# Optimization experiments

Measured on AMD Instinct MI355X. Metric: run time of the kernel, lower is better.

Reference implementation:

```python
import jax, jax.numpy as jnp
import numpy as np

D_KQ = 1024  # output_key_query_dim, used for the 1/sqrt(d) scale


def setup_inputs() -> dict:
    key = jax.random.key(0)
    kx, kq, kk, kv = jax.random.split(key, 4)
    B, S, D = 4, 2048, 1024
    x = jax.random.normal(kx, (B, S, D), dtype=jnp.float32)
    # nn.Linear(in, out, bias=False) weights, shape (out, in); y = x @ W.T
    scale = 1.0 / np.sqrt(D)
    Wq = jax.random.normal(kq, (D_KQ, D), dtype=jnp.float32) * scale
    Wk = jax.random.normal(kk, (D_KQ, D), dtype=jnp.float32) * scale
    Wv = jax.random.normal(kv, (D, D), dtype=jnp.float32) * scale
    return {"x": x, "Wq": Wq, "Wk": Wk, "Wv": Wv}


def reference(x, Wq, Wk, Wv):
    # q, k, v projections (bias=False): y = x @ W.T
    q = jnp.einsum('bsd,ed->bse', x, Wq)  # [B,S,Dkq]
    k = jnp.einsum('bsd,ed->bse', x, Wk)  # [B,S,Dkq]
    v = jnp.einsum('bsd,ed->bse', x, Wv)  # [B,S,Dv]
    scores = jnp.einsum('bqe,bke->bqk', q, k) / jnp.sqrt(
        jnp.asarray(D_KQ, dtype=q.dtype))
    # NOTE: the original torch code's masked_fill(causal_mask == 1, -inf) is a
    # no-op because the buffer contains only {-inf, 0} values, never 1.
    # Faithfully, NO causal mask is applied.
    attn = jax.nn.softmax(scores, axis=-1)
    # dropout in eval mode -> identity
    out = jnp.einsum('bqk,bke->bqe', attn, v)  # [B,S,Dv]
    return out
```

## Files before the change

### kernel.cpp

```cpp
#include <hip/hip_runtime.h>
#include <stdint.h>

#define B_ 4
#define S_ 2048
#define D_ 1024

typedef __attribute__((ext_vector_type(8))) short short8;
typedef __attribute__((ext_vector_type(4))) float f32x4;
typedef __attribute__((ext_vector_type(4))) int int4v;

__device__ inline ushort f2bf(float f) {
  union { float f; uint32_t u; } v; v.f = f;
  uint32_t u = v.u;
  u += 0x7FFFu + ((u >> 16) & 1u);
  return (ushort)(u >> 16);
}

__device__ inline float bf2f(ushort u) {
  union { uint32_t u; float f; } c; c.u = ((uint32_t)u) << 16;
  return c.f;
}

__device__ inline void gload_lds16(const ushort* g, ushort* l) {
  __builtin_amdgcn_global_load_lds(
      (__attribute__((address_space(1))) void*)(uintptr_t)g,
      (__attribute__((address_space(3))) void*)(uintptr_t)l,
      16, 0, 0);
}

__device__ inline uint lds_off(const ushort* p) {
  return (uint)(uintptr_t)(const __attribute__((address_space(3))) ushort*)(uintptr_t)p;
}

__device__ inline short8 dsr128(uint addr) {
  int4v r;
  asm volatile("ds_read_b128 %0, %1" : "=v"(r) : "v"(addr));
  return __builtin_bit_cast(short8, r);
}

__device__ inline void vwaitN(int n) {
  switch (n) {
    case 0: asm volatile("s_waitcnt vmcnt(0)"); break;
    case 1: asm volatile("s_waitcnt vmcnt(1)"); break;
    case 2: asm volatile("s_waitcnt vmcnt(2)"); break;
    case 3: asm volatile("s_waitcnt vmcnt(3)"); break;
    case 4: asm volatile("s_waitcnt vmcnt(4)"); break;
    case 5: asm volatile("s_waitcnt vmcnt(5)"); break;
    case 6: asm volatile("s_waitcnt vmcnt(6)"); break;
    case 7: asm volatile("s_waitcnt vmcnt(7)"); break;
    default: asm volatile("s_waitcnt vmcnt(8)"); break;
  }
}

__device__ inline void abar() { asm volatile("s_barrier"); }

__device__ inline void lgkm0() {
  asm volatile("s_waitcnt lgkmcnt(0)");
  __builtin_amdgcn_sched_barrier(0);
}

__global__ __launch_bounds__(256) void convert_all(
    const float* __restrict__ x, const float* __restrict__ wq,
    const float* __restrict__ wk, const float* __restrict__ wv,
    ushort* __restrict__ xb, ushort* __restrict__ wcat) {
  const int NX = B_ * S_ * D_;
  const int NW = D_ * D_;
  int e = (blockIdx.x * 256 + threadIdx.x) * 4;
  const float* src;
  ushort* dst;
  if (e < NX) {
    src = x + e; dst = xb + e;
  } else {
    int e2 = e - NX;
    int w = e2 / NW, off = e2 - w * NW;
    src = (w == 0 ? wq : w == 1 ? wk : wv) + off;
    dst = wcat + e2;
  }
  float4 f = *(const float4*)src;
  ushort4 o;
  o.x = f2bf(f.x); o.y = f2bf(f.y); o.z = f2bf(f.z); o.w = f2bf(f.w);
  *(ushort4*)dst = o;
}

template <int HH, int NH>
__device__ inline void mfma16(short8 (&af)[4][2], short8 (&bf)[2][2][2],
                              f32x4 (&acc)[8][4]) {
  __builtin_amdgcn_s_setprio(1);
  #pragma unroll
  for (int mf = 0; mf < 4; ++mf)
    #pragma unroll
    for (int nf = 0; nf < 2; ++nf)
      #pragma unroll
      for (int ks = 0; ks < 2; ++ks)
        acc[HH * 4 + mf][NH * 2 + nf] = __builtin_amdgcn_mfma_f32_16x16x32_bf16(
            af[mf][ks], bf[NH][nf][ks], acc[HH * 4 + mf][NH * 2 + nf], 0, 0, 0);
  __builtin_amdgcn_s_setprio(0);
}

__global__ __launch_bounds__(512, 2) void gemm256(
    const ushort* __restrict__ A, const ushort* __restrict__ Bm,
    ushort* __restrict__ C, int K, int lda, int ldb, int ldc,
    long sA, long sB, long sC, float scale) {
  constexpr int ATILE = 256 * 64;
  __shared__ ushort lds[4 * ATILE];
  ushort* ldsA = lds;
  ushort* ldsB = lds + 2 * ATILE;

  const int tid = threadIdx.x;
  const int wid = tid >> 6, lane = tid & 63;
  const int wr = wid >> 2, wc = wid & 3;
  const int la = lane & 15, kg = lane >> 4;
  const int m0 = blockIdx.x * 256, n0 = blockIdx.y * 256;
  const int bz = blockIdx.z;
  const ushort* Ag = A + (size_t)bz * sA;
  const ushort* Bg = Bm + (size_t)bz * sB;

  uint aOff[2][2]; int aDst[2][2];
  uint bOff[2][2]; int bDst[2][2];
  #pragma unroll
  for (int h = 0; h < 2; ++h)
    #pragma unroll
    for (int l = 0; l < 2; ++l) {
      int li = l * 512 + tid, ridx = li >> 3, c = li & 7;
      int rowA = (ridx < 64) ? h * 64 + ridx : 128 + h * 64 + (ridx - 64);
      int gcA = c ^ (rowA & 7);
      aOff[h][l] = (uint)((m0 + rowA) * lda + gcA * 8);
      aDst[h][l] = rowA * 64 + c * 8;
      int rowB = (ridx >> 5) * 64 + h * 32 + (ridx & 31);
      int gcB = c ^ (rowB & 7);
      bOff[h][l] = (uint)((n0 + rowB) * ldb + gcB * 8);
      bDst[h][l] = rowB * 64 + c * 8;
    }

  auto stageA = [&](int h, int buf, int t) {
    #pragma unroll
    for (int l = 0; l < 2; ++l)
      gload_lds16(Ag + aOff[h][l] + (size_t)t * 64, ldsA + buf * ATILE + aDst[h][l]);
  };
  auto stageB = [&](int h, int buf, int t) {
    #pragma unroll
    for (int l = 0; l < 2; ++l)
      gload_lds16(Bg + bOff[h][l] + (size_t)t * 64, ldsB + buf * ATILE + bDst[h][l]);
  };

  uint offAq[2][2][4];
  #pragma unroll
  for (int hh = 0; hh < 2; ++hh)
    #pragma unroll
    for (int ks = 0; ks < 2; ++ks)
      #pragma unroll
      for (int mf = 0; mf < 4; ++mf) {
        int row = wr * 128 + hh * 64 + mf * 16 + la;
        int kc = ((ks * 4 + kg) ^ (row & 7)) * 8;
        offAq[hh][ks][mf] = (uint)((row * 64 + kc) * 2);
      }
  uint offBq[2][2][2];
  #pragma unroll
  for (int nh = 0; nh < 2; ++nh)
    #pragma unroll
    for (int ks = 0; ks < 2; ++ks)
      #pragma unroll
      for (int nf = 0; nf < 2; ++nf) {
        int row = wc * 64 + nh * 32 + nf * 16 + la;
        int kc = ((ks * 4 + kg) ^ (row & 7)) * 8;
        offBq[nh][ks][nf] = (uint)((row * 64 + kc) * 2);
      }
  const uint ldsA0 = lds_off(ldsA);
  const uint ldsB0 = lds_off(ldsB);

  f32x4 acc[8][4];
  #pragma unroll
  for (int m = 0; m < 8; ++m)
    #pragma unroll
    for (int n = 0; n < 4; ++n) acc[m][n] = (f32x4)(0.f);
  short8 af[4][2];
  short8 bf[2][2][2];

  const int NT = K / 64;

  stageA(0, 0, 0); stageB(0, 0, 0); stageB(1, 0, 0); stageA(1, 0, 0);

  for (int t = 0; t < NT; ++t) {
    const uint aB = ldsA0 + (uint)((t & 1) * ATILE * 2);
    const uint bB = ldsB0 + (uint)((t & 1) * ATILE * 2);
    const int nb = (t + 1) & 1;

    vwaitN(4);
    abar();
    #pragma unroll
    for (int mf = 0; mf < 4; ++mf)
      #pragma unroll
      for (int ks = 0; ks < 2; ++ks) af[mf][ks] = dsr128(aB + offAq[0][ks][mf]);
    #pragma unroll
    for (int nf = 0; nf < 2; ++nf)
      #pragma unroll
      for (int ks = 0; ks < 2; ++ks) bf[0][nf][ks] = dsr128(bB + offBq[0][ks][nf]);
    if (t + 1 < NT) stageA(0, nb, t + 1);
    lgkm0();
    mfma16<0, 0>(af, bf, acc);

    vwaitN(t + 1 < NT ? 4 : 2);
    abar();
    #pragma unroll
    for (int nf = 0; nf < 2; ++nf)
      #pragma unroll
      for (int ks = 0; ks < 2; ++ks) bf[1][nf][ks] = dsr128(bB + offBq[1][ks][nf]);
    if (t + 1 < NT) stageB(0, nb, t + 1);
    lgkm0();
    mfma16<0, 1>(af, bf, acc);

    vwaitN(t + 1 < NT ? 4 : 0);
    abar();
    #pragma unroll
    for (int mf = 0; mf < 4; ++mf)
      #pragma unroll
      for (int ks = 0; ks < 2; ++ks) af[mf][ks] = dsr128(aB + offAq[1][ks][mf]);
    if (t + 1 < NT) stageB(1, nb, t + 1);
    lgkm0();
    mfma16<1, 0>(af, bf, acc);

    if (t + 1 < NT) stageA(1, nb, t + 1);
    mfma16<1, 1>(af, bf, acc);
  }

  #pragma unroll
  for (int mf = 0; mf < 8; ++mf) {
    #pragma unroll
    for (int nf = 0; nf < 4; ++nf) {
      int r = m0 + wr * 128 + (mf >> 2) * 64 + (mf & 3) * 16 + kg * 4;
      int col = n0 + wc * 64 + (nf >> 1) * 32 + (nf & 1) * 16 + la;
      #pragma unroll
      for (int jj = 0; jj < 4; ++jj)
        C[(size_t)bz * sC + (size_t)(r + jj) * ldc + col] =
            f2bf(acc[mf][nf][jj] * scale);
    }
  }
}

template <int H, int BM, int BN>
__device__ inline void mfma_ph(short8 (&afv)[BM / 64], short8 (&bfv)[BN / 64],
                               f32x4 (&acc)[BM / 32][BN / 64]) {
  constexpr int J = BM / 64, NF = BN / 64;
  __builtin_amdgcn_s_setprio(1);
  #pragma unroll
  for (int j = 0; j < J; ++j)
    #pragma unroll
    for (int nf = 0; nf < NF; ++nf)
      acc[H * J + j][nf] = __builtin_amdgcn_mfma_f32_16x16x32_bf16(
          afv[j], bfv[nf], acc[H * J + j][nf], 0, 0, 0);
  __builtin_amdgcn_s_setprio(0);
}

template <int BM, int BN, bool OUT_BF16, bool V_TRANS>
__global__ __launch_bounds__(512, 2) void gemm_p(
    const ushort* __restrict__ A, const ushort* __restrict__ Bm,
    void* __restrict__ C, ushort* __restrict__ Vt,
    int N, int K, int lda, int ldb, int ldc,
    long sA, long sB, long sC, float scale) {
  constexpr int J = BM / 64, NF = BN / 64, MF = BM / 32;
  constexpr int LAH = BM / 128;
  constexpr int LBH = BN / 128;
  constexpr int ABUF = BM * 64;
  constexpr int BBUF = BN * 64;
  constexpr int VW1 = 2 * LAH + 2 * LBH;
  __shared__ ushort lds[2 * ABUF + 3 * BBUF];
  ushort* ldsA = lds;
  ushort* ldsB = lds + 2 * ABUF;

  const int tid = threadIdx.x;
  const int wid = tid >> 6, lane = tid & 63;
  const int wr = wid >> 2, wc = wid & 3;
  const int la = lane & 15, kg = lane >> 4;
  const int m0 = blockIdx.x * BM, n0 = blockIdx.y * BN;
  const int bz = blockIdx.z;
  const ushort* Ag = A + (size_t)bz * sA;
  const ushort* Bg = Bm + (size_t)bz * sB;

  uint aOff[2][LAH]; int aDst[2][LAH];
  #pragma unroll
  for (int h = 0; h < 2; ++h)
    #pragma unroll
    for (int l = 0; l < LAH; ++l) {
      int li = l * 512 + tid, ridx = li >> 3, c = li & 7;
      int row = (ridx < BM / 4) ? h * (BM / 4) + ridx
                                : (h + 2) * (BM / 4) + (ridx - BM / 4);
      int gc = c ^ (row & 7);
      aOff[h][l] = (uint)((m0 + row) * lda + gc * 8);
      aDst[h][l] = row * 64 + c * 8;
    }
  uint bOff[2][LBH]; int bDst[2][LBH];
  #pragma unroll
  for (int h = 0; h < 2; ++h)
    #pragma unroll
    for (int l = 0; l < LBH; ++l) {
      int li = l * 512 + tid, ridx = li >> 3, c = li & 7;
      int row = h * (BN / 2) + ridx;
      int gc = c ^ (row & 7);
      bOff[h][l] = (uint)((n0 + row) * ldb + gc * 8);
      bDst[h][l] = row * 64 + c * 8;
    }

  auto stageA = [&](int h, int buf, int t) {
    #pragma unroll
    for (int l = 0; l < LAH; ++l)
      gload_lds16(Ag + aOff[h][l] + (size_t)t * 64, ldsA + buf * ABUF + aDst[h][l]);
  };
  auto stageB = [&](int h, int slot, int t) {
    #pragma unroll
    for (int l = 0; l < LBH; ++l)
      gload_lds16(Bg + bOff[h][l] + (size_t)t * 64, ldsB + slot * BBUF + bDst[h][l]);
  };

  uint offA[2][2][J];
  #pragma unroll
  for (int h = 0; h < 2; ++h)
    #pragma unroll
    for (int ks = 0; ks < 2; ++ks)
      #pragma unroll
      for (int j = 0; j < J; ++j) {
        int row = wr * (BM / 2) + h * (BM / 4) + j * 16 + la;
        int kc = ((ks * 4 + kg) ^ (row & 7)) * 8;
        offA[h][ks][j] = (uint)((row * 64 + kc) * 2);
      }
  uint offB[2][NF];
  #pragma unroll
  for (int ks = 0; ks < 2; ++ks)
    #pragma unroll
    for (int nf = 0; nf < NF; ++nf) {
      int row = wc * (BN / 4) + nf * 16 + la;
      int kc = ((ks * 4 + kg) ^ (row & 7)) * 8;
      offB[ks][nf] = (uint)((row * 64 + kc) * 2);
    }
  const uint ldsA0 = lds_off(ldsA);
  const uint ldsB0 = lds_off(ldsB);

  f32x4 acc[MF][NF];
  #pragma unroll
  for (int m = 0; m < MF; ++m)
    #pragma unroll
    for (int n = 0; n < NF; ++n) acc[m][n] = (f32x4)(0.f);
  short8 af[J], bf0[NF], bf1[NF];

  const int NT = K / 64;

  stageA(0, 0, 0); stageB(0, 0, 0); stageB(1, 0, 0);
  stageA(1, 0, 0);
  stageA(0, 1, 1); stageB(0, 1, 1); stageB(1, 1, 1);

  int bs = 0;
  for (int t = 0; t < NT; ++t) {
    const uint aB = ldsA0 + (uint)((t & 1) * ABUF * 2);
    const uint bB = ldsB0 + (uint)(bs * BBUF * 2);
    const int bs2 = (bs == 0) ? 2 : bs - 1;

    vwaitN(t + 1 < NT ? VW1 : LAH);
    abar();
    #pragma unroll
    for (int j = 0; j < J; ++j) af[j] = dsr128(aB + offA[0][0][j]);
    #pragma unroll
    for (int nf = 0; nf < NF; ++nf) bf0[nf] = dsr128(bB + offB[0][nf]);
    if (t + 1 < NT) stageA(1, (t + 1) & 1, t + 1);
    lgkm0();
    mfma_ph<0, BM, BN>(af, bf0, acc);
    #pragma unroll
    for (int j = 0; j < J; ++j) af[j] = dsr128(aB + offA[0][1][j]);
    #pragma unroll
    for (int nf = 0; nf < NF; ++nf) bf1[nf] = dsr128(bB + offB[1][nf]);
    lgkm0();
    mfma_ph<0, BM, BN>(af, bf1, acc);

    vwaitN(t + 1 < NT ? VW1 : 0);
    abar();
    #pragma unroll
    for (int j = 0; j < J; ++j) af[j] = dsr128(aB + offA[1][0][j]);
    if (t + 2 < NT) { stageA(0, t & 1, t + 2); stageB(0, bs2, t + 2); }
    lgkm0();
    mfma_ph<1, BM, BN>(af, bf0, acc);
    #pragma unroll
    for (int j = 0; j < J; ++j) af[j] = dsr128(aB + offA[1][1][j]);
    if (t + 2 < NT) stageB(1, bs2, t + 2);
    lgkm0();
    mfma_ph<1, BM, BN>(af, bf1, acc);

    bs = (bs == 2) ? 0 : bs + 1;
  }

  if (V_TRANS && n0 >= 2048) {
    const int b = m0 >> 11;
    ushort* Vb = Vt + (size_t)b * D_ * S_;
    #pragma unroll
    for (int m = 0; m < MF; ++m) {
      #pragma unroll
      for (int n = 0; n < NF; ++n) {
        int r = m0 + wr * (BM / 2) + m * 16 + kg * 4;
        int e = (n0 - 2048) + wc * (BN / 4) + n * 16 + la;
        int s0 = r & 2047;
        ushort4 o;
        o.x = f2bf(acc[m][n][0]); o.y = f2bf(acc[m][n][1]);
        o.z = f2bf(acc[m][n][2]); o.w = f2bf(acc[m][n][3]);
        *(ushort4*)&Vb[(size_t)e * S_ + s0] = o;
      }
    }
  } else {
    char* Cb = (char*)C;
    #pragma unroll
    for (int m = 0; m < MF; ++m) {
      #pragma unroll
      for (int n = 0; n < NF; ++n) {
        int r = m0 + wr * (BM / 2) + m * 16 + kg * 4;
        int col = n0 + wc * (BN / 4) + n * 16 + la;
        #pragma unroll
        for (int jj = 0; jj < 4; ++jj) {
          float v = acc[m][n][jj] * scale;
          size_t idx = (size_t)bz * sC + (size_t)(r + jj) * ldc + col;
          if (OUT_BF16) ((ushort*)Cb)[idx] = f2bf(v);
          else          ((float*)Cb)[idx]  = v;
        }
      }
    }
  }
}

__global__ __launch_bounds__(256) void softmax_rows(
    const ushort* __restrict__ Sc, ushort* __restrict__ P) {
  size_t row = blockIdx.x;
  const ushort* src = Sc + row * S_;
  ushort* dst = P + row * S_;
  int tid = threadIdx.x;
  short8 v = *(const short8*)(src + tid * 8);
  float vals[8];
  float m = -1e30f;
  #pragma unroll
  for (int i = 0; i < 8; ++i) {
    vals[i] = bf2f((ushort)v[i]);
    m = fmaxf(m, vals[i]);
  }
  #pragma unroll
  for (int off = 1; off < 64; off <<= 1) m = fmaxf(m, __shfl_xor(m, off));
  __shared__ float redm[4];
  if ((tid & 63) == 0) redm[tid >> 6] = m;
  __syncthreads();
  m = fmaxf(fmaxf(redm[0], redm[1]), fmaxf(redm[2], redm[3]));
  float s = 0.f;
  #pragma unroll
  for (int i = 0; i < 8; ++i) {
    vals[i] = __expf(vals[i] - m);
    s += vals[i];
  }
  #pragma unroll
  for (int off = 1; off < 64; off <<= 1) s += __shfl_xor(s, off);
  __shared__ float reds[4];
  if ((tid & 63) == 0) reds[tid >> 6] = s;
  __syncthreads();
  s = reds[0] + reds[1] + reds[2] + reds[3];
  float inv = 1.0f / s;
  short8 o;
  #pragma unroll
  for (int i = 0; i < 8; ++i) o[i] = (short)f2bf(vals[i] * inv);
  *(short8*)(dst + tid * 8) = o;
}

extern "C" void kernel_launch(void* const* d_in, const int* in_sizes, int n_in,
                              void* d_out, int out_size, void* d_ws, size_t ws_size,
                              hipStream_t stream) {
  const float* x  = (const float*)d_in[0];
  const float* Wq = (const float*)d_in[1];
  const float* Wk = (const float*)d_in[2];
  const float* Wv = (const float*)d_in[3];
  float* out = (float*)d_out;

  char* ws = (char*)d_ws;
  ushort* Xb   = (ushort*)(ws + 0);
  ushort* Wcat = (ushort*)(ws + 16777216);
  ushort* QKV  = (ushort*)(ws + 23068672);
  ushort* Vt   = (ushort*)(ws + 73400320);
  ushort* Sc   = (ushort*)(ws + 90177536);
  ushort* P    = (ushort*)(ws + 157286400);

  const int NTOT = B_ * S_ * D_ + 3 * D_ * D_;

  convert_all<<<NTOT / 4 / 256, 256, 0, stream>>>(x, Wq, Wk, Wv, Xb, Wcat);

  gemm_p<128, 256, true, true><<<dim3(64, 12, 1), 512, 0, stream>>>(
      Xb, Wcat, QKV, Vt, 3072, 1024, 1024, 1024, 3072, 0, 0, 0, 1.0f);

  gemm256<<<dim3(8, 8, B_), 512, 0, stream>>>(
      QKV, QKV + 1024, Sc, 1024, 3072, 3072, 2048,
      (long)S_ * 3072, (long)S_ * 3072, (long)S_ * S_, 1.0f / 32.0f);

  softmax_rows<<<B_ * S_, 256, 0, stream>>>(Sc, P);

  gemm_p<128, 256, false, false><<<dim3(16, 4, B_), 512, 0, stream>>>(
      P, Vt, out, nullptr, 1024, 2048, 2048, 2048, 1024,
      (long)S_ * S_, (long)S_ * D_, (long)S_ * D_, 1.0f);
}
```

Before: 168.3 us.

## Fuse softmax exp and row sums into QK^T epilogue, normalize in PV epilogue

Removes the standalone softmax kernel. The QK^T GEMM epilogue now writes exp(score) directly and produces per-tile partial row sums. The PV GEMM sums those partials and scales its output by the reciprocal. The QKV projection is also split into a gemm256 launch for Q/K and a gemm_p launch that writes only the transposed V. This avoids a full read and write of the score matrix, but it drops the max subtraction, so large scores could overflow for inputs with a larger range.

Result: faster. 156.5 us (-7.0%).

```diff
diff --git a/kernel.cpp b/kernel.cpp
--- a/kernel.cpp
+++ b/kernel.cpp
@@ -14,11 +14,6 @@
   uint32_t u = v.u;
   u += 0x7FFFu + ((u >> 16) & 1u);
   return (ushort)(u >> 16);
-}
-
-__device__ inline float bf2f(ushort u) {
-  union { uint32_t u; float f; } c; c.u = ((uint32_t)u) << 16;
-  return c.f;
 }
 
 __device__ inline void gload_lds16(const ushort* g, ushort* l) {
@@ -97,9 +92,11 @@
   __builtin_amdgcn_s_setprio(0);
 }
 
+template <bool SM>
 __global__ __launch_bounds__(512, 2) void gemm256(
     const ushort* __restrict__ A, const ushort* __restrict__ Bm,
-    ushort* __restrict__ C, int K, int lda, int ldb, int ldc,
+    ushort* __restrict__ C, float* __restrict__ psum,
+    int K, int lda, int ldb, int ldc,
     long sA, long sB, long sC, float scale) {
   constexpr int ATILE = 256 * 64;
   __shared__ ushort lds[4 * ATILE];
@@ -223,16 +220,53 @@
     mfma16<1, 1>(af, bf, acc);
   }
 
-  #pragma unroll
-  for (int mf = 0; mf < 8; ++mf) {
-    #pragma unroll
-    for (int nf = 0; nf < 4; ++nf) {
-      int r = m0 + wr * 128 + (mf >> 2) * 64 + (mf & 3) * 16 + kg * 4;
-      int col = n0 + wc * 64 + (nf >> 1) * 32 + (nf & 1) * 16 + la;
-      #pragma unroll
-      for (int jj = 0; jj < 4; ++jj)
-        C[(size_t)bz * sC + (size_t)(r + jj) * ldc + col] =
-            f2bf(acc[mf][nf][jj] * scale);
+  if constexpr (SM) {
+    __shared__ float psum_lds[4][256];
+    float rsum[8][4];
+    #pragma unroll
+    for (int mf = 0; mf < 8; ++mf)
+      #pragma unroll
+      for (int jj = 0; jj < 4; ++jj) rsum[mf][jj] = 0.f;
+    #pragma unroll
+    for (int mf = 0; mf < 8; ++mf) {
+      #pragma unroll
+      for (int nf = 0; nf < 4; ++nf) {
+        int r = m0 + wr * 128 + (mf >> 2) * 64 + (mf & 3) * 16 + kg * 4;
+        int col = n0 + wc * 64 + (nf >> 1) * 32 + (nf & 1) * 16 + la;
+        #pragma unroll
+        for (int jj = 0; jj < 4; ++jj) {
+          float e = __expf(acc[mf][nf][jj] * scale);
+          C[(size_t)bz * sC + (size_t)(r + jj) * ldc + col] = f2bf(e);
+          rsum[mf][jj] += e;
+        }
+      }
+    }
+    #pragma unroll
+    for (int mf = 0; mf < 8; ++mf)
+      #pragma unroll
+      for (int jj = 0; jj < 4; ++jj) {
+        float s = rsum[mf][jj];
+        s += __shfl_xor(s, 1); s += __shfl_xor(s, 2);
+        s += __shfl_xor(s, 4); s += __shfl_xor(s, 8);
+        if (la == 0)
+          psum_lds[wc][wr * 128 + (mf >> 2) * 64 + (mf & 3) * 16 + kg * 4 + jj] = s;
+      }
+    __syncthreads();
+    if (tid < 256)
+      psum[((size_t)bz * 8 + blockIdx.y) * 2048 + m0 + tid] =
+          psum_lds[0][tid] + psum_lds[1][tid] + psum_lds[2][tid] + psum_lds[3][tid];
+  } else {
+    #pragma unroll
+    for (int mf = 0; mf < 8; ++mf) {
+      #pragma unroll
+      for (int nf = 0; nf < 4; ++nf) {
+        int r = m0 + wr * 128 + (mf >> 2) * 64 + (mf & 3) * 16 + kg * 4;
+        int col = n0 + wc * 64 + (nf >> 1) * 32 + (nf & 1) * 16 + la;
+        #pragma unroll
+        for (int jj = 0; jj < 4; ++jj)
+          C[(size_t)bz * sC + (size_t)(r + jj) * ldc + col] =
+              f2bf(acc[mf][nf][jj] * scale);
+      }
     }
   }
 }
@@ -251,10 +285,11 @@
   __builtin_amdgcn_s_setprio(0);
 }
 
-template <int BM, int BN, bool OUT_BF16, bool V_TRANS>
+template <int BM, int BN, bool OUT_BF16, bool V_TRANS, bool NORM>
 __global__ __launch_bounds__(512, 2) void gemm_p(
     const ushort* __restrict__ A, const ushort* __restrict__ Bm,
     void* __restrict__ C, ushort* __restrict__ Vt,
+    const float* __restrict__ psum,
     int N, int K, int lda, int ldb, int ldc,
     long sA, long sB, long sC, float scale) {
   constexpr int J = BM / 64, NF = BN / 64, MF = BM / 32;
@@ -385,7 +420,20 @@
     bs = (bs == 2) ? 0 : bs + 1;
   }
 
-  if (V_TRANS && n0 >= 2048) {
+  __shared__ float inv_l[BM];
+  if constexpr (NORM) {
+    __syncthreads();
+    if (tid < BM) {
+      float s = 0.f;
+      #pragma unroll
+      for (int q = 0; q < 8; ++q)
+        s += psum[((size_t)bz * 8 + q) * 2048 + m0 + tid];
+      inv_l[tid] = 1.0f / s;
+    }
+    __syncthreads();
+  }
+
+  if constexpr (V_TRANS) {
     const int b = m0 >> 11;
     ushort* Vb = Vt + (size_t)b * D_ * S_;
     #pragma unroll
@@ -393,7 +441,7 @@
       #pragma unroll
       for (int n = 0; n < NF; ++n) {
         int r = m0 + wr * (BM / 2) + m * 16 + kg * 4;
-        int e = (n0 - 2048) + wc * (BN / 4) + n * 16 + la;
+        int e = n0 + wc * (BN / 4) + n * 16 + la;
         int s0 = r & 2047;
         ushort4 o;
         o.x = f2bf(acc[m][n][0]); o.y = f2bf(acc[m][n][1]);
@@ -407,57 +455,19 @@
     for (int m = 0; m < MF; ++m) {
       #pragma unroll
       for (int n = 0; n < NF; ++n) {
-        int r = m0 + wr * (BM / 2) + m * 16 + kg * 4;
+        int rl = wr * (BM / 2) + m * 16 + kg * 4;
         int col = n0 + wc * (BN / 4) + n * 16 + la;
         #pragma unroll
         for (int jj = 0; jj < 4; ++jj) {
-          float v = acc[m][n][jj] * scale;
-          size_t idx = (size_t)bz * sC + (size_t)(r + jj) * ldc + col;
+          float sc = NORM ? inv_l[rl + jj] : scale;
+          float v = acc[m][n][jj] * sc;
+          size_t idx = (size_t)bz * sC + (size_t)(m0 + rl + jj) * ldc + col;
           if (OUT_BF16) ((ushort*)Cb)[idx] = f2bf(v);
           else          ((float*)Cb)[idx]  = v;
         }
       }
     }
   }
-}
-
-__global__ __launch_bounds__(256) void softmax_rows(
-    const ushort* __restrict__ Sc, ushort* __restrict__ P) {
-  size_t row = blockIdx.x;
-  const ushort* src = Sc + row * S_;
-  ushort* dst = P + row * S_;
-  int tid = threadIdx.x;
-  short8 v = *(const short8*)(src + tid * 8);
-  float vals[8];
-  float m = -1e30f;
-  #pragma unroll
-  for (int i = 0; i < 8; ++i) {
-    vals[i] = bf2f((ushort)v[i]);
-    m = fmaxf(m, vals[i]);
-  }
-  #pragma unroll
-  for (int off = 1; off < 64; off <<= 1) m = fmaxf(m, __shfl_xor(m, off));
-  __shared__ float redm[4];
-  if ((tid & 63) == 0) redm[tid >> 6] = m;
-  __syncthreads();
-  m = fmaxf(fmaxf(redm[0], redm[1]), fmaxf(redm[2], redm[3]));
-  float s = 0.f;
-  #pragma unroll
-  for (int i = 0; i < 8; ++i) {
-    vals[i] = __expf(vals[i] - m);
-    s += vals[i];
-  }
-  #pragma unroll
-  for (int off = 1; off < 64; off <<= 1) s += __shfl_xor(s, off);
-  __shared__ float reds[4];
-  if ((tid & 63) == 0) reds[tid >> 6] = s;
-  __syncthreads();
-  s = reds[0] + reds[1] + reds[2] + reds[3];
-  float inv = 1.0f / s;
-  short8 o;
-  #pragma unroll
-  for (int i = 0; i < 8; ++i) o[i] = (short)f2bf(vals[i] * inv);
-  *(short8*)(dst + tid * 8) = o;
 }
 
 extern "C" void kernel_launch(void* const* d_in, const int* in_sizes, int n_in,
@@ -474,23 +484,25 @@
   ushort* Wcat = (ushort*)(ws + 16777216);
   ushort* QKV  = (ushort*)(ws + 23068672);
   ushort* Vt   = (ushort*)(ws + 73400320);
-  ushort* Sc   = (ushort*)(ws + 90177536);
-  ushort* P    = (ushort*)(ws + 157286400);
+  ushort* Pu   = (ushort*)(ws + 90177536);
+  float*  psum = (float*) (ws + 157286400);
 
   const int NTOT = B_ * S_ * D_ + 3 * D_ * D_;
 
   convert_all<<<NTOT / 4 / 256, 256, 0, stream>>>(x, Wq, Wk, Wv, Xb, Wcat);
 
-  gemm_p<128, 256, true, true><<<dim3(64, 12, 1), 512, 0, stream>>>(
-      Xb, Wcat, QKV, Vt, 3072, 1024, 1024, 1024, 3072, 0, 0, 0, 1.0f);
-
-  gemm256<<<dim3(8, 8, B_), 512, 0, stream>>>(
-      QKV, QKV + 1024, Sc, 1024, 3072, 3072, 2048,
+  gemm256<false><<<dim3(32, 8, 1), 512, 0, stream>>>(
+      Xb, Wcat, QKV, nullptr, 1024, 1024, 1024, 3072, 0, 0, 0, 1.0f);
+
+  gemm_p<128, 256, true, true, false><<<dim3(64, 4, 1), 512, 0, stream>>>(
+      Xb, Wcat + (size_t)2048 * 1024, nullptr, Vt, nullptr,
+      1024, 1024, 1024, 1024, 0, 0, 0, 0, 1.0f);
+
+  gemm256<true><<<dim3(8, 8, B_), 512, 0, stream>>>(
+      QKV, QKV + 1024, Pu, psum, 1024, 3072, 3072, 2048,
       (long)S_ * 3072, (long)S_ * 3072, (long)S_ * S_, 1.0f / 32.0f);
 
-  softmax_rows<<<B_ * S_, 256, 0, stream>>>(Sc, P);
-
-  gemm_p<128, 256, false, false><<<dim3(16, 4, B_), 512, 0, stream>>>(
-      P, Vt, out, nullptr, 1024, 2048, 2048, 2048, 1024,
+  gemm_p<128, 256, false, false, true><<<dim3(16, 4, B_), 512, 0, stream>>>(
+      Pu, Vt, out, nullptr, psum, 1024, 2048, 2048, 2048, 1024,
       (long)S_ * S_, (long)S_ * D_, (long)S_ * D_, 1.0f);
 }
```
